# Optimization experiments

Hardware: AMD Instinct MI355X
Metric: run time of the kernel (lower is better)

Reference implementation:

```python
import jax, jax.numpy as jnp
import numpy as np
import math

B, T, F_ = 4, 1024, 1024
TO_DIM, FROM_DIM, LATENT, H = 1024, 1024, 1024, 16
HEAD_DIM = LATENT // H

def _linear_params(key, in_dim, out_dim):
    kw, kb = jax.random.split(key)
    bound = 1.0 / math.sqrt(in_dim)
    W = jax.random.uniform(kw, (out_dim, in_dim), minval=-bound, maxval=bound, dtype=jnp.float32)
    b = jax.random.uniform(kb, (out_dim,), minval=-bound, maxval=bound, dtype=jnp.float32)
    return W, b

def setup_inputs() -> dict:
    key = jax.random.key(0)
    ks = jax.random.split(key, 7)
    X_to = jax.random.normal(ks[0], (B, T, TO_DIM), dtype=jnp.float32)
    X_from = jax.random.normal(ks[1], (B, F_, FROM_DIM), dtype=jnp.float32)
    mask_from = jax.random.randint(ks[2], (B, T, F_), 0, 2, dtype=jnp.int32)
    Wq, bq = _linear_params(ks[3], TO_DIM, LATENT)
    Wk, bk = _linear_params(ks[4], FROM_DIM, LATENT)
    Wv, bv = _linear_params(ks[5], FROM_DIM, LATENT)
    Wo, bo = _linear_params(ks[6], LATENT, TO_DIM)
    return {"X_to": X_to, "X_from": X_from, "mask_from": mask_from,
            "Wq": Wq, "bq": bq, "Wk": Wk, "bk": bk, "Wv": Wv, "bv": bv, "Wo": Wo, "bo": bo}

def _split_heads(x):
    # [b, t, (h k)] -> [b, h, t, k]
    b, t, _ = x.shape
    return x.reshape(b, t, H, HEAD_DIM).transpose(0, 2, 1, 3)

def reference(X_to, X_from, mask_from, Wq, bq, Wk, bk, Wv, bv, Wo, bo):
    Q = _split_heads(X_to @ Wq.T + bq)
    # NOTE: source swaps names — K comes from v_linear, V from k_linear. Reproduced literally.
    K = _split_heads(X_from @ Wv.T + bv)
    V = _split_heads(X_from @ Wk.T + bk)
    attn = jnp.einsum('bhtk,bhfk->bhtf', Q, K) / math.sqrt(HEAD_DIM)
    attn = jnp.where(mask_from[:, None, :, :] == 0, jnp.float32(-10000.0), attn)
    attn = jax.nn.softmax(attn, axis=-1)
    out = jnp.einsum('bhtf,bhfk->bhtk', attn, V)  # [b,h,t,k]
    out = out.transpose(0, 2, 1, 3).reshape(X_to.shape[0], X_to.shape[1], LATENT)
    return out @ Wo.T + bo
```

## Files before the change

kernel.cpp:

```cpp
#include <hip/hip_runtime.h>
#include <hip/hip_bf16.h>
#include <math.h>

#define BB 4
#define TT 1024
#define FF 1024
#define DIM 1024
#define NH 16
#define HD 64
#define MROWS (BB * TT)
#define FB (FF / 64)

typedef __attribute__((ext_vector_type(8))) short short8;
typedef __attribute__((ext_vector_type(4))) float f32x4;
typedef __hip_bfloat16 bf16;

__device__ __forceinline__ void async_copy16(const void* g, void* l) {
    __builtin_amdgcn_global_load_lds((const __attribute__((address_space(1))) void*)g,
                                     (__attribute__((address_space(3))) void*)l,
                                     16, 0, 0);
}

struct ConvArgs {
    const float* src[6];
    bf16* dst[6];
    int nvec[6];
    int blk_end[6];
    const int* mask;
    unsigned long long* Mb;
};

__global__ __launch_bounds__(256) void convert_pack(ConvArgs a) {
    int bx = blockIdx.x;
    if (bx >= a.blk_end[5]) {
        const int lane = threadIdx.x & 63;
        const int waveId = (bx - a.blk_end[5]) * 4 + (threadIdx.x >> 6);
#pragma unroll
        for (int it = 0; it < 16; ++it) {
            int c = waveId * 16 + it;
            int v = a.mask[(size_t)c * 64 + lane];
            unsigned long long bits = __ballot(v != 0);
            if (lane == 0) a.Mb[c] = bits;
        }
        return;
    }
    int seg = 0;
#pragma unroll
    for (int k = 0; k < 5; ++k) if (bx >= a.blk_end[k]) seg = k + 1;
    int b0 = seg ? a.blk_end[seg - 1] : 0;
    int idx = (bx - b0) * 256 + threadIdx.x;
    if (idx >= a.nvec[seg]) return;
    float4 v = ((const float4*)a.src[seg])[idx];
    union { bf16 t[4]; ushort4 u; } o;
    o.t[0] = __float2bfloat16(v.x);
    o.t[1] = __float2bfloat16(v.y);
    o.t[2] = __float2bfloat16(v.z);
    o.t[3] = __float2bfloat16(v.w);
    *(ushort4*)(a.dst[seg] + 4 * (size_t)idx) = o.u;
}

#define BK 64

struct QkvArgs {
    const bf16* A[3]; const bf16* W[3]; const float* bias[3]; bf16* C[3];
    int N[3]; int biasRow[3];
};

__global__ __launch_bounds__(256) void gemm_qkv(QkvArgs q) {
    __shared__ bf16 smem[128 * 132];
    bf16* As = smem;
    bf16* Bs = smem + 128 * BK;

    const int op = blockIdx.z;
    const bf16* A = q.A[op];
    const bf16* W = q.W[op];
    const float* bias = q.bias[op];
    bf16* C = q.C[op];
    const int N = q.N[op];
    const int brow = q.biasRow[op];

    int m0, n0;
    if (brow) { m0 = blockIdx.x * 128; n0 = blockIdx.y * 128; }
    else      { n0 = blockIdx.x * 128; m0 = blockIdx.y * 128; }

    const int tid  = threadIdx.x;
    const int lane = tid & 63;
    const int wave = tid >> 6;
    const int quad = lane >> 4;
    const int l16  = lane & 15;
    const int wm = wave & 1;
    const int wn = wave >> 1;
    const int wbase = tid & ~63;

    f32x4 acc[4][4] = {};

    for (int k0 = 0; k0 < DIM; k0 += BK) {
#pragma unroll
        for (int j = 0; j < 4; ++j) {
            int slot = j * 256 + tid;
            int r = slot >> 3;
            int g = (slot & 7) ^ (r & 7);
            async_copy16(A + (size_t)(m0 + r) * DIM + k0 + g * 8,
                         As + (size_t)(j * 256 + wbase) * 8);
            async_copy16(W + (size_t)(n0 + r) * DIM + k0 + g * 8,
                         Bs + (size_t)(j * 256 + wbase) * 8);
        }
        __syncthreads();

#pragma unroll
        for (int kk = 0; kk < 2; ++kk) {
            short8 a[4], b[4];
#pragma unroll
            for (int mi = 0; mi < 4; ++mi) {
                int r = wm * 64 + mi * 16 + l16;
                int p = (kk * 4 + quad) ^ (r & 7);
                a[mi] = *(const short8*)(As + r * BK + p * 8);
            }
#pragma unroll
            for (int ni = 0; ni < 4; ++ni) {
                int r = wn * 64 + ni * 16 + l16;
                int p = (kk * 4 + quad) ^ (r & 7);
                b[ni] = *(const short8*)(Bs + r * BK + p * 8);
            }
#pragma unroll
            for (int mi = 0; mi < 4; ++mi)
#pragma unroll
                for (int ni = 0; ni < 4; ++ni)
                    acc[mi][ni] = __builtin_amdgcn_mfma_f32_16x16x32_bf16(
                        a[mi], b[ni], acc[mi][ni], 0, 0, 0);
        }
        __syncthreads();
    }

    bf16* Cs = smem;
#pragma unroll
    for (int ni = 0; ni < 4; ++ni) {
        const int nl = wn * 64 + ni * 16 + l16;
        float bcol = brow ? 0.0f : bias[n0 + nl];
#pragma unroll
        for (int mi = 0; mi < 4; ++mi)
#pragma unroll
            for (int i = 0; i < 4; ++i) {
                const int ml = wm * 64 + mi * 16 + quad * 4 + i;
                float v = acc[mi][ni][i] + (brow ? bias[m0 + ml] : bcol);
                Cs[ml * 132 + nl] = __float2bfloat16(v);
            }
    }
    __syncthreads();
#pragma unroll
    for (int j = 0; j < 8; ++j) {
        int slot = j * 256 + tid;
        int rr = slot >> 4, cc = slot & 15;
        short8 v = *(const short8*)(Cs + rr * 132 + cc * 8);
        *(short8*)(C + (size_t)(m0 + rr) * N + n0 + cc * 8) = v;
    }
}

__global__ __launch_bounds__(256) void gemm_o(
    const bf16* __restrict__ A, const bf16* __restrict__ W,
    const float* __restrict__ bias, float* __restrict__ C)
{
    __shared__ float smemf[128 * 66];
    bf16* As = (bf16*)smemf;
    bf16* Bs = As + 128 * BK;

    const int n0 = blockIdx.x * 64;
    const int m0 = blockIdx.y * 128;
    const int tid  = threadIdx.x;
    const int lane = tid & 63;
    const int wave = tid >> 6;
    const int quad = lane >> 4;
    const int l16  = lane & 15;
    const int wm = wave & 1;
    const int wn = wave >> 1;
    const int wbase = tid & ~63;

    f32x4 acc[4][2] = {};

    for (int k0 = 0; k0 < DIM; k0 += BK) {
#pragma unroll
        for (int j = 0; j < 4; ++j) {
            int slot = j * 256 + tid;
            int r = slot >> 3;
            int g = (slot & 7) ^ (r & 7);
            async_copy16(A + (size_t)(m0 + r) * DIM + k0 + g * 8,
                         As + (size_t)(j * 256 + wbase) * 8);
        }
#pragma unroll
        for (int j = 0; j < 2; ++j) {
            int slot = j * 256 + tid;
            int r = slot >> 3;
            int g = (slot & 7) ^ (r & 7);
            async_copy16(W + (size_t)(n0 + r) * DIM + k0 + g * 8,
                         Bs + (size_t)(j * 256 + wbase) * 8);
        }
        __syncthreads();

#pragma unroll
        for (int kk = 0; kk < 2; ++kk) {
            short8 a[4], b[2];
#pragma unroll
            for (int mi = 0; mi < 4; ++mi) {
                int r = wm * 64 + mi * 16 + l16;
                int p = (kk * 4 + quad) ^ (r & 7);
                a[mi] = *(const short8*)(As + r * BK + p * 8);
            }
#pragma unroll
            for (int ni = 0; ni < 2; ++ni) {
                int r = wn * 32 + ni * 16 + l16;
                int p = (kk * 4 + quad) ^ (r & 7);
                b[ni] = *(const short8*)(Bs + r * BK + p * 8);
            }
#pragma unroll
            for (int mi = 0; mi < 4; ++mi)
#pragma unroll
                for (int ni = 0; ni < 2; ++ni)
                    acc[mi][ni] = __builtin_amdgcn_mfma_f32_16x16x32_bf16(
                        a[mi], b[ni], acc[mi][ni], 0, 0, 0);
        }
        __syncthreads();
    }

    float* Cs = smemf;
#pragma unroll
    for (int ni = 0; ni < 2; ++ni) {
        const int nl = wn * 32 + ni * 16 + l16;
        const float bcol = bias[n0 + nl];
#pragma unroll
        for (int mi = 0; mi < 4; ++mi)
#pragma unroll
            for (int i = 0; i < 4; ++i) {
                const int ml = wm * 64 + mi * 16 + quad * 4 + i;
                Cs[ml * 66 + nl] = acc[mi][ni][i] + bcol;
            }
    }
    __syncthreads();
#pragma unroll
    for (int j = 0; j < 8; ++j) {
        int slot = j * 256 + tid;
        int rr = slot >> 4, cc = slot & 15;
        float4 v = *(const float4*)(Cs + rr * 66 + cc * 4);
        *(float4*)(C + (size_t)(m0 + rr) * DIM + n0 + cc * 4) = v;
    }
}

__global__ __launch_bounds__(256) void attn_kernel(
    const bf16* Qg, const bf16* __restrict__ Kg, const bf16* __restrict__ Vtg,
    const unsigned long long* __restrict__ Mbits, bf16* Og)
{
    __shared__ bf16 Ks[64 * 64];
    __shared__ bf16 Vts[64 * 64];
    __shared__ bf16 Ps[64 * 72];

    const int tid  = threadIdx.x;
    const int lane = tid & 63;
    const int wave = tid >> 6;
    const int quad = lane >> 4;
    const int l16  = lane & 15;
    const int t0 = blockIdx.x * 64;
    const int h  = blockIdx.y;
    const int b  = blockIdx.z;
    const size_t qrow0 = (size_t)b * TT + t0;
    const size_t krow0 = (size_t)b * FF;
    const int wbase = tid & ~63;

    const bf16* qptr = Qg + (qrow0 + wave * 16 + l16) * DIM + h * HD;
    short8 qa0 = *(const short8*)(qptr + quad * 8);
    short8 qa1 = *(const short8*)(qptr + 32 + quad * 8);

    float lrow[4] = {0.f, 0.f, 0.f, 0.f};
    f32x4 oacc[4] = {};

    for (int f0 = 0; f0 < FF; f0 += 64) {
        const int fb = f0 >> 6;
#pragma unroll
        for (int j = 0; j < 2; ++j) {
            int slot = j * 256 + tid;
            int r = slot >> 3;
            int blk = (slot & 7) ^ (r & 7);
            async_copy16(Kg + (krow0 + f0 + r) * DIM + h * HD + blk * 8,
                         Ks + (size_t)(j * 256 + wbase) * 8);
            async_copy16(Vtg + (size_t)(h * HD + r) * MROWS + b * FF + f0 + blk * 8,
                         Vts + (size_t)(j * 256 + wbase) * 8);
        }
        __syncthreads();

        f32x4 sacc[4] = {};
#pragma unroll
        for (int nt = 0; nt < 4; ++nt) {
            int r = nt * 16 + l16;
            short8 kb0 = *(const short8*)(Ks + r * 64 + ((quad       ^ (r & 7)) * 8));
            short8 kb1 = *(const short8*)(Ks + r * 64 + (((quad + 4) ^ (r & 7)) * 8));
            sacc[nt] = __builtin_amdgcn_mfma_f32_16x16x32_bf16(qa0, kb0, sacc[nt], 0, 0, 0);
            sacc[nt] = __builtin_amdgcn_mfma_f32_16x16x32_bf16(qa1, kb1, sacc[nt], 0, 0, 0);
        }

#pragma unroll
        for (int i = 0; i < 4; ++i) {
            const int prow = wave * 16 + quad * 4 + i;
            unsigned long long m64 = Mbits[(qrow0 + prow) * FB + fb];
            unsigned long long sh = m64 >> l16;
            unsigned lo = (unsigned)sh, hi = (unsigned)(sh >> 32);
            float p0 = (lo & 1u)         ? __expf(sacc[0][i] * 0.125f) : 0.f;
            float p1 = ((lo >> 16) & 1u) ? __expf(sacc[1][i] * 0.125f) : 0.f;
            float p2 = (hi & 1u)         ? __expf(sacc[2][i] * 0.125f) : 0.f;
            float p3 = ((hi >> 16) & 1u) ? __expf(sacc[3][i] * 0.125f) : 0.f;
            lrow[i] += p0 + p1 + p2 + p3;
            Ps[prow * 72 +  0 + l16] = __float2bfloat16(p0);
            Ps[prow * 72 + 16 + l16] = __float2bfloat16(p1);
            Ps[prow * 72 + 32 + l16] = __float2bfloat16(p2);
            Ps[prow * 72 + 48 + l16] = __float2bfloat16(p3);
        }

        short8 pa0 = *(const short8*)(Ps + (wave * 16 + l16) * 72 + quad * 8);
        short8 pa1 = *(const short8*)(Ps + (wave * 16 + l16) * 72 + 32 + quad * 8);
#pragma unroll
        for (int nt = 0; nt < 4; ++nt) {
            int r = nt * 16 + l16;
            short8 vb0 = *(const short8*)(Vts + r * 64 + ((quad       ^ (r & 7)) * 8));
            short8 vb1 = *(const short8*)(Vts + r * 64 + (((quad + 4) ^ (r & 7)) * 8));
            oacc[nt] = __builtin_amdgcn_mfma_f32_16x16x32_bf16(pa0, vb0, oacc[nt], 0, 0, 0);
            oacc[nt] = __builtin_amdgcn_mfma_f32_16x16x32_bf16(pa1, vb1, oacc[nt], 0, 0, 0);
        }
        __syncthreads();
    }

#pragma unroll
    for (int i = 0; i < 4; ++i) {
        float l = lrow[i];
        l += __shfl_xor(l, 1);
        l += __shfl_xor(l, 2);
        l += __shfl_xor(l, 4);
        l += __shfl_xor(l, 8);
        float inv = 1.0f / l;
        const int prow = wave * 16 + quad * 4 + i;
#pragma unroll
        for (int nt = 0; nt < 4; ++nt)
            Ps[prow * 72 + nt * 16 + l16] = __float2bfloat16(oacc[nt][i] * inv);
    }
    __syncthreads();
#pragma unroll
    for (int j = 0; j < 2; ++j) {
        int s = j * 256 + tid;
        int rr = s >> 3, off = (s & 7) * 8;
        short8 v = *(const short8*)(Ps + rr * 72 + off);
        *(short8*)(Og + (qrow0 + rr) * DIM + h * HD + off) = v;
    }
}

extern "C" void kernel_launch(void* const* d_in, const int* in_sizes, int n_in,
                              void* d_out, int out_size, void* d_ws, size_t ws_size,
                              hipStream_t stream) {
    const float* X_to   = (const float*)d_in[0];
    const float* X_from = (const float*)d_in[1];
    const int*   mask   = (const int*)  d_in[2];
    const float* Wq     = (const float*)d_in[3];
    const float* bq     = (const float*)d_in[4];
    const float* Wk     = (const float*)d_in[5];
    const float* bk     = (const float*)d_in[6];
    const float* Wv     = (const float*)d_in[7];
    const float* bv     = (const float*)d_in[8];
    const float* Wo     = (const float*)d_in[9];
    const float* bo     = (const float*)d_in[10];
    float* out = (float*)d_out;

    char* ws = (char*)d_ws;
    bf16* Xt16 = (bf16*)(ws);
    bf16* Xf16 = (bf16*)(ws + (8u  << 20));
    bf16* Wq16 = (bf16*)(ws + (16u << 20));
    bf16* Wv16 = (bf16*)(ws + (18u << 20));
    bf16* Wk16 = (bf16*)(ws + (20u << 20));
    bf16* Wo16 = (bf16*)(ws + (22u << 20));
    bf16* Q16  = (bf16*)(ws + (24u << 20));
    bf16* K16  = (bf16*)(ws + (32u << 20));
    bf16* Vt16 = (bf16*)(ws + (40u << 20));
    unsigned long long* Mb = (unsigned long long*)(ws + (48u << 20));

    ConvArgs ca;
    ca.src[0] = X_to;   ca.dst[0] = Xt16; ca.nvec[0] = MROWS * DIM / 4;
    ca.src[1] = X_from; ca.dst[1] = Xf16; ca.nvec[1] = MROWS * DIM / 4;
    ca.src[2] = Wq;     ca.dst[2] = Wq16; ca.nvec[2] = DIM * DIM / 4;
    ca.src[3] = Wv;     ca.dst[3] = Wv16; ca.nvec[3] = DIM * DIM / 4;
    ca.src[4] = Wk;     ca.dst[4] = Wk16; ca.nvec[4] = DIM * DIM / 4;
    ca.src[5] = Wo;     ca.dst[5] = Wo16; ca.nvec[5] = DIM * DIM / 4;
    int cum = 0;
    for (int k = 0; k < 6; ++k) { cum += ca.nvec[k] / 256; ca.blk_end[k] = cum; }
    ca.mask = mask; ca.Mb = Mb;
    convert_pack<<<cum + 1024, 256, 0, stream>>>(ca);

    QkvArgs qa;
    qa.A[0] = Xt16; qa.W[0] = Wq16; qa.bias[0] = bq; qa.C[0] = Q16;
    qa.N[0] = DIM; qa.biasRow[0] = 0;
    qa.A[1] = Xf16; qa.W[1] = Wv16; qa.bias[1] = bv; qa.C[1] = K16;
    qa.N[1] = DIM; qa.biasRow[1] = 0;
    qa.A[2] = Wk16; qa.W[2] = Xf16; qa.bias[2] = bk; qa.C[2] = Vt16;
    qa.N[2] = MROWS; qa.biasRow[2] = 1;
    gemm_qkv<<<dim3(8, 32, 3), 256, 0, stream>>>(qa);

    attn_kernel<<<dim3(TT / 64, NH, BB), 256, 0, stream>>>(
        Q16, K16, Vt16, Mb, Q16);

    gemm_o<<<dim3(DIM / 64, MROWS / 128), 256, 0, stream>>>(Q16, Wo16, bo, out);
}
```

Before: 233.6 us.

## Remap blocks to XCDs for L2 locality and widen attention key tile to 128

The QKV, output-projection and attention kernels now remap the linear block index so that blocks sharing the same operand rows (the same batch-head in attention, the same M or N panels in the GEMMs) land on the same XCD, which should improve L2 reuse. The attention kernel also processes 128 keys per iteration instead of 64. This halves the number of barrier-separated loop trips and issues more MFMAs per sync, at the cost of more LDS and more registers per block (eight score accumulators). The remapping assumes the fixed grid shapes.

Measured after the change: 240.2 us. 1.03x slower.

```diff
diff --git a/kernel.cpp b/kernel.cpp
--- a/kernel.cpp
+++ b/kernel.cpp
@@ -79,9 +79,17 @@
     const int N = q.N[op];
     const int brow = q.biasRow[op];
 
+    const int lin = blockIdx.x + 8 * blockIdx.y;
+    const int xcd = lin & 7;
+    const int t   = lin >> 3;
     int m0, n0;
-    if (brow) { m0 = blockIdx.x * 128; n0 = blockIdx.y * 128; }
-    else      { n0 = blockIdx.x * 128; m0 = blockIdx.y * 128; }
+    if (brow) {
+        m0 = (((t & 7) + xcd) & 7) * 128;
+        n0 = (xcd * 4 + (t >> 3)) * 128;
+    } else {
+        m0 = (xcd * 4 + (t >> 3)) * 128;
+        n0 = (((t & 7) + xcd) & 7) * 128;
+    }
 
     const int tid  = threadIdx.x;
     const int lane = tid & 63;
@@ -164,8 +172,12 @@
     bf16* As = (bf16*)smemf;
     bf16* Bs = As + 128 * BK;
 
-    const int n0 = blockIdx.x * 64;
-    const int m0 = blockIdx.y * 128;
+    const int lin = blockIdx.x + 16 * blockIdx.y;
+    const int xcd = lin & 7;
+    const int t   = lin >> 3;
+    const int m0 = (xcd * 4 + (t >> 4)) * 128;
+    const int n0 = (((t & 15) + 2 * xcd) & 15) * 64;
+
     const int tid  = threadIdx.x;
     const int lane = tid & 63;
     const int wave = tid >> 6;
@@ -248,18 +260,24 @@
     const bf16* Qg, const bf16* __restrict__ Kg, const bf16* __restrict__ Vtg,
     const unsigned long long* __restrict__ Mbits, bf16* Og)
 {
-    __shared__ bf16 Ks[64 * 64];
-    __shared__ bf16 Vts[64 * 64];
-    __shared__ bf16 Ps[64 * 72];
+    __shared__ bf16 Ks[128 * 64];
+    __shared__ bf16 Vts[64 * 128];
+    __shared__ bf16 Ps[64 * 136];
 
     const int tid  = threadIdx.x;
     const int lane = tid & 63;
     const int wave = tid >> 6;
     const int quad = lane >> 4;
     const int l16  = lane & 15;
-    const int t0 = blockIdx.x * 64;
-    const int h  = blockIdx.y;
-    const int b  = blockIdx.z;
+
+    const int lin = blockIdx.x + 16 * (blockIdx.y + 16 * blockIdx.z);
+    const int xcd = lin & 7;
+    const int t   = lin >> 3;
+    const int bh  = xcd * 8 + (t >> 4);
+    const int b   = bh >> 4;
+    const int h   = bh & 15;
+    const int t0  = (t & 15) * 64;
+
     const size_t qrow0 = (size_t)b * TT + t0;
     const size_t krow0 = (size_t)b * FF;
     const int wbase = tid & ~63;
@@ -271,23 +289,24 @@
     float lrow[4] = {0.f, 0.f, 0.f, 0.f};
     f32x4 oacc[4] = {};
 
-    for (int f0 = 0; f0 < FF; f0 += 64) {
-        const int fb = f0 >> 6;
-#pragma unroll
-        for (int j = 0; j < 2; ++j) {
+    for (int f0 = 0; f0 < FF; f0 += 128) {
+#pragma unroll
+        for (int j = 0; j < 4; ++j) {
             int slot = j * 256 + tid;
-            int r = slot >> 3;
-            int blk = (slot & 7) ^ (r & 7);
-            async_copy16(Kg + (krow0 + f0 + r) * DIM + h * HD + blk * 8,
+            int rk = slot >> 3;
+            int gk = (slot & 7) ^ (rk & 7);
+            async_copy16(Kg + (krow0 + f0 + rk) * DIM + h * HD + gk * 8,
                          Ks + (size_t)(j * 256 + wbase) * 8);
-            async_copy16(Vtg + (size_t)(h * HD + r) * MROWS + b * FF + f0 + blk * 8,
+            int rv = slot >> 4;
+            int gv = (slot & 15) ^ (rv & 15);
+            async_copy16(Vtg + (size_t)(h * HD + rv) * MROWS + b * FF + f0 + gv * 8,
                          Vts + (size_t)(j * 256 + wbase) * 8);
         }
         __syncthreads();
 
-        f32x4 sacc[4] = {};
-#pragma unroll
-        for (int nt = 0; nt < 4; ++nt) {
+        f32x4 sacc[8] = {};
+#pragma unroll
+        for (int nt = 0; nt < 8; ++nt) {
             int r = nt * 16 + l16;
             short8 kb0 = *(const short8*)(Ks + r * 64 + ((quad       ^ (r & 7)) * 8));
             short8 kb1 = *(const short8*)(Ks + r * 64 + (((quad + 4) ^ (r & 7)) * 8));
@@ -298,29 +317,37 @@
 #pragma unroll
         for (int i = 0; i < 4; ++i) {
             const int prow = wave * 16 + quad * 4 + i;
-            unsigned long long m64 = Mbits[(qrow0 + prow) * FB + fb];
-            unsigned long long sh = m64 >> l16;
-            unsigned lo = (unsigned)sh, hi = (unsigned)(sh >> 32);
-            float p0 = (lo & 1u)         ? __expf(sacc[0][i] * 0.125f) : 0.f;
-            float p1 = ((lo >> 16) & 1u) ? __expf(sacc[1][i] * 0.125f) : 0.f;
-            float p2 = (hi & 1u)         ? __expf(sacc[2][i] * 0.125f) : 0.f;
-            float p3 = ((hi >> 16) & 1u) ? __expf(sacc[3][i] * 0.125f) : 0.f;
-            lrow[i] += p0 + p1 + p2 + p3;
-            Ps[prow * 72 +  0 + l16] = __float2bfloat16(p0);
-            Ps[prow * 72 + 16 + l16] = __float2bfloat16(p1);
-            Ps[prow * 72 + 32 + l16] = __float2bfloat16(p2);
-            Ps[prow * 72 + 48 + l16] = __float2bfloat16(p3);
-        }
-
-        short8 pa0 = *(const short8*)(Ps + (wave * 16 + l16) * 72 + quad * 8);
-        short8 pa1 = *(const short8*)(Ps + (wave * 16 + l16) * 72 + 32 + quad * 8);
+#pragma unroll
+            for (int half = 0; half < 2; ++half) {
+                unsigned long long m64 = Mbits[(qrow0 + prow) * FB + (f0 >> 6) + half];
+                unsigned long long sh = m64 >> l16;
+                unsigned lo = (unsigned)sh, hi = (unsigned)(sh >> 32);
+                const int sb = half * 4;
+                float p0 = (lo & 1u)         ? __expf(sacc[sb + 0][i] * 0.125f) : 0.f;
+                float p1 = ((lo >> 16) & 1u) ? __expf(sacc[sb + 1][i] * 0.125f) : 0.f;
+                float p2 = (hi & 1u)         ? __expf(sacc[sb + 2][i] * 0.125f) : 0.f;
+                float p3 = ((hi >> 16) & 1u) ? __expf(sacc[sb + 3][i] * 0.125f) : 0.f;
+                lrow[i] += p0 + p1 + p2 + p3;
+                Ps[prow * 136 + half * 64 +  0 + l16] = __float2bfloat16(p0);
+                Ps[prow * 136 + half * 64 + 16 + l16] = __float2bfloat16(p1);
+                Ps[prow * 136 + half * 64 + 32 + l16] = __float2bfloat16(p2);
+                Ps[prow * 136 + half * 64 + 48 + l16] = __float2bfloat16(p3);
+            }
+        }
+
+        short8 pa[4];
+#pragma unroll
+        for (int kf = 0; kf < 4; ++kf)
+            pa[kf] = *(const short8*)(Ps + (wave * 16 + l16) * 136 + kf * 32 + quad * 8);
 #pragma unroll
         for (int nt = 0; nt < 4; ++nt) {
-            int r = nt * 16 + l16;
-            short8 vb0 = *(const short8*)(Vts + r * 64 + ((quad       ^ (r & 7)) * 8));
-            short8 vb1 = *(const short8*)(Vts + r * 64 + (((quad + 4) ^ (r & 7)) * 8));
-            oacc[nt] = __builtin_amdgcn_mfma_f32_16x16x32_bf16(pa0, vb0, oacc[nt], 0, 0, 0);
-            oacc[nt] = __builtin_amdgcn_mfma_f32_16x16x32_bf16(pa1, vb1, oacc[nt], 0, 0, 0);
+            int rd = nt * 16 + l16;
+#pragma unroll
+            for (int kf = 0; kf < 4; ++kf) {
+                int g = (kf * 4 + quad) ^ (rd & 15);
+                short8 vb = *(const short8*)(Vts + rd * 128 + g * 8);
+                oacc[nt] = __builtin_amdgcn_mfma_f32_16x16x32_bf16(pa[kf], vb, oacc[nt], 0, 0, 0);
+            }
         }
         __syncthreads();
     }
@@ -336,14 +363,14 @@
         const int prow = wave * 16 + quad * 4 + i;
 #pragma unroll
         for (int nt = 0; nt < 4; ++nt)
-            Ps[prow * 72 + nt * 16 + l16] = __float2bfloat16(oacc[nt][i] * inv);
+            Ps[prow * 136 + nt * 16 + l16] = __float2bfloat16(oacc[nt][i] * inv);
     }
     __syncthreads();
 #pragma unroll
     for (int j = 0; j < 2; ++j) {
         int s = j * 256 + tid;
         int rr = s >> 3, off = (s & 7) * 8;
-        short8 v = *(const short8*)(Ps + rr * 72 + off);
+        short8 v = *(const short8*)(Ps + rr * 136 + off);
         *(short8*)(Og + (qrow0 + rr) * DIM + h * HD + off) = v;
     }
 }
```
